# Kernel optimization log

Measured on AMD Instinct MI355X. Metric: run time of the kernel, lower is better.

## Reference

```python
import jax, jax.numpy as jnp
import numpy as np

E = 16      # number of encoders
L = 3       # RNN blocks per encoder
D_IN = 32   # input feature dim
D = 512     # RNN state dim
H_FF = 2048 # encoder FFNN hidden
D_ENC = 512 # encoder output dim
N_DEC = 4   # decoder layers
H_DEC = 2048
D_OUT = 1024
T = 128     # sequence length


def setup_inputs() -> dict:
    key = jax.random.key(0)
    ks = jax.random.split(key, 16)
    def s(k, shape, fan):
        return jax.random.normal(k, shape, jnp.float32) / np.sqrt(fan).astype(np.float32)
    return {
        "x": jax.random.normal(ks[0], (1, T, D_IN), jnp.float32),
        "W_in0": s(ks[1], (E, D_IN, D), D_IN),
        "Wh0": s(ks[2], (E, D, D), D),
        "b0": jnp.zeros((E, D), jnp.float32),
        "W_in_rest": s(ks[3], (E, L - 1, D, D), D),
        "Wh_rest": s(ks[4], (E, L - 1, D, D), D),
        "b_rest": jnp.zeros((E, L - 1, D), jnp.float32),
        "W_ff1": s(ks[5], (E, L * D, H_FF), L * D),
        "b_ff1": jnp.zeros((E, H_FF), jnp.float32),
        "W_ff2": s(ks[6], (E, H_FF, D_ENC), H_FF),
        "b_ff2": jnp.zeros((E, D_ENC), jnp.float32),
        "W_d0": s(ks[7], (E * D_ENC, H_DEC), E * D_ENC),
        "b_d0": jnp.zeros((H_DEC,), jnp.float32),
        "W_dmid": s(ks[8], (N_DEC - 2, H_DEC, H_DEC), H_DEC),
        "b_dmid": jnp.zeros((N_DEC - 2, H_DEC), jnp.float32),
        "W_dout": s(ks[9], (H_DEC, D_OUT), H_DEC),
        "b_dout": jnp.zeros((D_OUT,), jnp.float32),
    }


def reference(x, W_in0, Wh0, b0, W_in_rest, Wh_rest, b_rest,
              W_ff1, b_ff1, W_ff2, b_ff2,
              W_d0, b_d0, W_dmid, b_dmid, W_dout, b_dout):
    def step(h, x_t):
        # h: [E, L, D] stacked-RNN states for all 16 encoders; x_t: [D_IN]
        h0 = jnp.tanh(jnp.einsum('i,eid->ed', x_t, W_in0)
                      + jnp.einsum('ed,edk->ek', h[:, 0], Wh0) + b0)
        hs = [h0]
        for l in range(1, L):  # chain blocks: input = previous block's new state
            hl = jnp.tanh(jnp.einsum('ed,edk->ek', hs[-1], W_in_rest[:, l - 1])
                          + jnp.einsum('ed,edk->ek', h[:, l], Wh_rest[:, l - 1])
                          + b_rest[:, l - 1])
            hs.append(hl)
        h_new = jnp.stack(hs, axis=1)                    # [E, L, D]
        cat = h_new.reshape(E, L * D)                    # cat(states, dim=-1)
        ff = jax.nn.gelu(jnp.einsum('ef,efh->eh', cat, W_ff1) + b_ff1)
        enc_out = jnp.einsum('eh,ehk->ek', ff, W_ff2) + b_ff2  # [E, D_ENC]
        # decoder over concatenated encoder outputs
        z = jnp.tanh(enc_out.reshape(-1) @ W_d0 + b_d0)
        for i in range(N_DEC - 2):
            z = jnp.tanh(z @ W_dmid[i] + b_dmid[i])
        y = z @ W_dout + b_dout                          # [D_OUT]
        return h_new, y

    h_init = jnp.zeros((E, L, D), x.dtype)
    _, ys = jax.lax.scan(step, h_init, x[0])             # [T, D_OUT]
    return ys[None]                                      # [1, T, D_OUT]
```

## Files before the change

kernel.cpp:

```cpp
#include <hip/hip_runtime.h>
#include <hip/hip_bf16.h>
#include <hip/hip_fp16.h>

#define E_ 16
#define T_ 128

typedef _Float16 h2_t __attribute__((ext_vector_type(2)));

__device__ __forceinline__ float fdot2u(uint32_t w, uint32_t h, float acc) {
#if __has_builtin(__builtin_amdgcn_fdot2)
  return __builtin_amdgcn_fdot2(__builtin_bit_cast(h2_t, w),
                                __builtin_bit_cast(h2_t, h), acc, false);
#else
  h2_t wv = __builtin_bit_cast(h2_t, w), hv = __builtin_bit_cast(h2_t, h);
  return acc + (float)wv.x * (float)hv.x + (float)wv.y * (float)hv.y;
#endif
}

__device__ __forceinline__ uint32_t rdlane(uint32_t v, int l) {
  return (uint32_t)__builtin_amdgcn_readlane((int)v, l);
}

__device__ __forceinline__ uint32_t packh2(float a, float b) {
  h2_t p; p.x = (_Float16)a; p.y = (_Float16)b;
  return __builtin_bit_cast(uint32_t, p);
}

__device__ __forceinline__ float apply_act(float v, int act) {
  if (act == 1) return tanhf(v);
  if (act == 2) {
    const float c = 0.7978845608028654f;
    return 0.5f * v * (1.0f + tanhf(c * (v + 0.044715f * v * v * v)));
  }
  return v;
}

__global__ void __launch_bounds__(256) gemm_skinny(
    const float* __restrict__ A, const float* __restrict__ W,
    const float* __restrict__ bias, float* __restrict__ C, float* __restrict__ part,
    int N, int K, int lda, int ldc,
    long sAe, long sWe, long sBe, long sCe,
    int S, int act)
{
  int n0 = blockIdx.x * 64;
  int e  = blockIdx.y;
  int s  = blockIdx.z;
  const float* Ae = A + (long)e * sAe;
  const float* We = W + (long)e * sWe + n0;
  int kper = K / S;
  int kb = s * kper, ke = kb + kper;

  __shared__ float As[32][132];
  __shared__ float Ws[32][68];
  int tid = threadIdx.x;
  int tn = tid & 15, tm = tid >> 4;
  float acc[8][4];
  #pragma unroll
  for (int i = 0; i < 8; ++i)
    #pragma unroll
    for (int j = 0; j < 4; ++j) acc[i][j] = 0.f;

  for (int k0 = kb; k0 < ke; k0 += 32) {
    #pragma unroll
    for (int i = 0; i < 4; ++i) {
      int li = i * 1024 + tid * 4;
      int r = li >> 5, kk = li & 31;
      float4 a4 = *(const float4*)(Ae + (long)r * lda + k0 + kk);
      As[kk+0][r] = a4.x; As[kk+1][r] = a4.y; As[kk+2][r] = a4.z; As[kk+3][r] = a4.w;
    }
    #pragma unroll
    for (int i = 0; i < 2; ++i) {
      int li = i * 1024 + tid * 4;
      int kk = li >> 6, j = li & 63;
      *(float4*)&Ws[kk][j] = *(const float4*)(We + (long)(k0 + kk) * N + j);
    }
    __syncthreads();
    #pragma unroll
    for (int kk = 0; kk < 32; ++kk) {
      float4 a0 = *(const float4*)&As[kk][tm*8];
      float4 a1 = *(const float4*)&As[kk][tm*8+4];
      float4 w4 = *(const float4*)&Ws[kk][tn*4];
      float av[8] = {a0.x,a0.y,a0.z,a0.w,a1.x,a1.y,a1.z,a1.w};
      float wv[4] = {w4.x,w4.y,w4.z,w4.w};
      #pragma unroll
      for (int i2 = 0; i2 < 8; ++i2)
        #pragma unroll
        for (int j2 = 0; j2 < 4; ++j2)
          acc[i2][j2] = fmaf(av[i2], wv[j2], acc[i2][j2]);
    }
    __syncthreads();
  }

  if (S == 1) {
    #pragma unroll
    for (int i2 = 0; i2 < 8; ++i2) {
      int r = tm * 8 + i2;
      float4 o; float* op = (float*)&o;
      #pragma unroll
      for (int j2 = 0; j2 < 4; ++j2)
        op[j2] = apply_act(acc[i2][j2] + bias[(long)e*sBe + n0 + tn*4 + j2], act);
      *(float4*)(C + (long)e*sCe + (long)r*ldc + n0 + tn*4) = o;
    }
  } else {
    float* pp = part + ((long)(s * gridDim.y + e) * 128) * N;
    #pragma unroll
    for (int i2 = 0; i2 < 8; ++i2) {
      int r = tm * 8 + i2;
      float4 o; float* op = (float*)&o;
      #pragma unroll
      for (int j2 = 0; j2 < 4; ++j2) op[j2] = acc[i2][j2];
      *(float4*)(pp + (long)r * N + n0 + tn*4) = o;
    }
  }
}

__global__ void __launch_bounds__(256) reduce_ep(
    const float* __restrict__ part, const float* __restrict__ bias, float* __restrict__ C,
    int S, int N, int ldc, long sBe, long sCe, int act, int total, int Eb)
{
  int idx = blockIdx.x * 256 + threadIdx.x;
  if (idx >= total) return;
  int n = idx % N;
  int r = (idx / N) & 127;
  int e = idx / (N * 128);
  long sstride = (long)Eb * 128 * N;
  float v = 0.f;
  for (int s = 0; s < S; ++s) v += part[s * sstride + ((long)e * 128 + r) * N + n];
  v = apply_act(v + bias[(long)e * sBe + n], act);
  C[(long)e * sCe + (long)r * ldc + n] = v;
}

#define RNN_NV 46
#define RNN_NG 9

__global__ void
__attribute__((amdgpu_flat_work_group_size(1024, 1024)))
__attribute__((amdgpu_waves_per_eu(4, 4)))
__attribute__((amdgpu_num_vgpr(128)))
rnn_seq(
    const float* __restrict__ P,
    const float* __restrict__ Wh,
    float* __restrict__ H,
    long sWe)
{
  __shared__ uint32_t lw[RNN_NG * 4096];
  __shared__ uint32_t hbuf[256];
  __shared__ float    red[3 * 512];

  int tid  = threadIdx.x;
  int lane = tid & 63;
  int wid  = tid >> 6;
  int kq   = wid >> 2;
  int colg = wid & 3;
  int c0   = colg * 128 + lane * 2;
  int e    = blockIdx.x;

  const float* W = Wh + (long)e * sWe;

  uint32_t w0[RNN_NV], w1[RNN_NV];
  #pragma unroll
  for (int q = 0; q < RNN_NV; ++q) {
    int k = kq * 128 + 2 * q;
    float2 ra = *(const float2*)(W + (long)k * 512 + c0);
    float2 rb = *(const float2*)(W + (long)(k + 1) * 512 + c0);
    w0[q] = packh2(ra.x, rb.x);
    w1[q] = packh2(ra.y, rb.y);
  }
  for (int g = 0; g < RNN_NG; ++g) {
    int k = kq * 128 + 2 * (RNN_NV + 2 * g);
    float2 ra = *(const float2*)(W + (long)(k + 0) * 512 + c0);
    float2 rb = *(const float2*)(W + (long)(k + 1) * 512 + c0);
    float2 rc = *(const float2*)(W + (long)(k + 2) * 512 + c0);
    float2 rd = *(const float2*)(W + (long)(k + 3) * 512 + c0);
    uint4 v;
    v.x = packh2(ra.x, rb.x);
    v.y = packh2(ra.y, rb.y);
    v.z = packh2(rc.x, rd.x);
    v.w = packh2(rc.y, rd.y);
    *(uint4*)(lw + ((long)g * 1024 + tid) * 4) = v;
  }
  if (tid < 256) hbuf[tid] = 0;
  __syncthreads();

  for (int t = 0; t < T_; ++t) {
    float2 pv = make_float2(0.f, 0.f);
    if (kq == 0) pv = *(const float2*)(P + ((long)t * E_ + e) * 512 + c0);
    uint32_t hr = hbuf[kq * 64 + lane];
    float a0 = 0.f, a1 = 0.f;
    #pragma unroll
    for (int L = 0; L < RNN_NV; ++L) {
      uint32_t hb = rdlane(hr, L);
      a0 = fdot2u(w0[L], hb, a0);
      a1 = fdot2u(w1[L], hb, a1);
    }
    #pragma unroll
    for (int g = 0; g < RNN_NG; ++g) {
      uint4 v = *(const uint4*)(lw + (g * 1024 + tid) * 4);
      uint32_t hb0 = rdlane(hr, RNN_NV + 2 * g);
      uint32_t hb1 = rdlane(hr, RNN_NV + 2 * g + 1);
      a0 = fdot2u(v.x, hb0, a0);
      a1 = fdot2u(v.y, hb0, a1);
      a0 = fdot2u(v.z, hb1, a0);
      a1 = fdot2u(v.w, hb1, a1);
    }
    if (kq) *(float2*)(red + (kq - 1) * 512 + c0) = make_float2(a0, a1);
    __syncthreads();
    if (kq == 0) {
      float v0 = a0 + red[c0]     + red[512 + c0]     + red[1024 + c0]     + pv.x;
      float v1 = a1 + red[c0 + 1] + red[512 + c0 + 1] + red[1024 + c0 + 1] + pv.y;
      v0 = tanhf(v0); v1 = tanhf(v1);
      *(float2*)(H + ((long)t * E_ + e) * 1536 + c0) = make_float2(v0, v1);
      hbuf[colg * 64 + lane] = packh2(v0, v1);
    }
    __syncthreads();
  }
}

extern "C" void kernel_launch(void* const* d_in, const int* in_sizes, int n_in,
                              void* d_out, int out_size, void* d_ws, size_t ws_size,
                              hipStream_t stream)
{
  const float* x      = (const float*)d_in[0];
  const float* W_in0  = (const float*)d_in[1];
  const float* Wh0    = (const float*)d_in[2];
  const float* b0     = (const float*)d_in[3];
  const float* W_inr  = (const float*)d_in[4];
  const float* Wh_r   = (const float*)d_in[5];
  const float* b_r    = (const float*)d_in[6];
  const float* W_ff1  = (const float*)d_in[7];
  const float* b_ff1  = (const float*)d_in[8];
  const float* W_ff2  = (const float*)d_in[9];
  const float* b_ff2  = (const float*)d_in[10];
  const float* W_d0   = (const float*)d_in[11];
  const float* b_d0   = (const float*)d_in[12];
  const float* W_dmid = (const float*)d_in[13];
  const float* b_dmid = (const float*)d_in[14];
  const float* W_dout = (const float*)d_in[15];
  const float* b_dout = (const float*)d_in[16];
  float* ws = (float*)d_ws;

  float* h    = ws;
  float* P    = ws + 3145728;
  float* FF   = ws + 4194304;
  float* ENC  = ws + 8388608;
  float* Z0   = ws + 9437184;
  float* Z1   = ws + 9699328;
  float* Z2   = ws + 9961472;
  float* PART = ws + 10223616;

  (void)in_sizes; (void)n_in; (void)out_size; (void)ws_size;

  dim3 blk(256);

  gemm_skinny<<<dim3(8,16,1), blk, 0, stream>>>(x, W_in0, b0, P, PART,
      512, 32, 32, 8192, 0L, 16384L, 512L, 512L, 1, 0);
  rnn_seq<<<dim3(16), dim3(1024), 0, stream>>>(P, Wh0, h, 262144L);
  gemm_skinny<<<dim3(8,16,1), blk, 0, stream>>>(h, W_inr, b_r, P, PART,
      512, 512, 24576, 8192, 1536L, 524288L, 1024L, 512L, 1, 0);
  rnn_seq<<<dim3(16), dim3(1024), 0, stream>>>(P, Wh_r, h + 512, 524288L);
  gemm_skinny<<<dim3(8,16,1), blk, 0, stream>>>(h + 512, W_inr + 262144, b_r + 512, P, PART,
      512, 512, 24576, 8192, 1536L, 524288L, 1024L, 512L, 1, 0);
  rnn_seq<<<dim3(16), dim3(1024), 0, stream>>>(P, Wh_r + 262144, h + 1024, 524288L);
  gemm_skinny<<<dim3(32,16,1), blk, 0, stream>>>(h, W_ff1, b_ff1, FF, PART,
      2048, 1536, 24576, 32768, 1536L, 3145728L, 2048L, 2048L, 1, 2);
  gemm_skinny<<<dim3(8,16,2), blk, 0, stream>>>(FF, W_ff2, b_ff2, ENC, PART,
      512, 2048, 32768, 8192, 2048L, 1048576L, 512L, 512L, 2, 0);
  reduce_ep<<<dim3(4096), blk, 0, stream>>>(PART, b_ff2, ENC,
      2, 512, 8192, 512L, 512L, 0, 16*128*512, 16);
  gemm_skinny<<<dim3(32,1,8), blk, 0, stream>>>(ENC, W_d0, b_d0, Z0, PART,
      2048, 8192, 8192, 2048, 0L, 0L, 0L, 0L, 8, 0);
  reduce_ep<<<dim3(1024), blk, 0, stream>>>(PART, b_d0, Z0,
      8, 2048, 2048, 0L, 0L, 1, 128*2048, 1);
  gemm_skinny<<<dim3(32,1,8), blk, 0, stream>>>(Z0, W_dmid, b_dmid, Z1, PART,
      2048, 2048, 2048, 2048, 0L, 0L, 0L, 0L, 8, 0);
  reduce_ep<<<dim3(1024), blk, 0, stream>>>(PART, b_dmid, Z1,
      8, 2048, 2048, 0L, 0L, 1, 128*2048, 1);
  gemm_skinny<<<dim3(32,1,8), blk, 0, stream>>>(Z1, W_dmid + 4194304, b_dmid + 2048, Z2, PART,
      2048, 2048, 2048, 2048, 0L, 0L, 0L, 0L, 8, 0);
  reduce_ep<<<dim3(1024), blk, 0, stream>>>(PART, b_dmid + 2048, Z2,
      8, 2048, 2048, 0L, 0L, 1, 128*2048, 1);
  gemm_skinny<<<dim3(16,1,8), blk, 0, stream>>>(Z2, W_dout, b_dout, (float*)d_out, PART,
      1024, 2048, 2048, 1024, 0L, 0L, 0L, 0L, 8, 0);
  reduce_ep<<<dim3(512), blk, 0, stream>>>(PART, b_dout, (float*)d_out,
      8, 1024, 1024, 0L, 0L, 0, 128*1024, 1);
}
```

Baseline: 1.400 ms.

## Replace FP32 SIMT skinny GEMM with FP16 MFMA 16x16x32 tiles

Rewrites the batched skinny GEMM to use MFMA f32_16x16x32_f16 instructions. Activations are converted to fp16 and staged in shared memory, while weights are loaded straight from global memory, converted per lane, and no longer staged. Each block now covers a 128x128 tile with four waves of 64x64, so the grid's x dimension is halved. This targets the FP32 FMA cost of the encoder/decoder GEMMs. It costs fp16 rounding of the inputs, plus strided uncoalesced weight loads and scalar output stores.

```diff
diff --git a/kernel.cpp b/kernel.cpp
--- a/kernel.cpp
+++ b/kernel.cpp
@@ -6,6 +6,9 @@
 #define T_ 128
 
 typedef _Float16 h2_t __attribute__((ext_vector_type(2)));
+typedef _Float16 half4_t __attribute__((ext_vector_type(4)));
+typedef _Float16 half8_t __attribute__((ext_vector_type(8)));
+typedef float f32x4 __attribute__((ext_vector_type(4)));
 
 __device__ __forceinline__ float fdot2u(uint32_t w, uint32_t h, float acc) {
 #if __has_builtin(__builtin_amdgcn_fdot2)
@@ -35,82 +38,92 @@
   return v;
 }
 
-__global__ void __launch_bounds__(256) gemm_skinny(
+__global__ void __launch_bounds__(256) gemm_mfma(
     const float* __restrict__ A, const float* __restrict__ W,
     const float* __restrict__ bias, float* __restrict__ C, float* __restrict__ part,
     int N, int K, int lda, int ldc,
     long sAe, long sWe, long sBe, long sCe,
     int S, int act)
 {
-  int n0 = blockIdx.x * 64;
+  int n0 = blockIdx.x * 128;
   int e  = blockIdx.y;
   int s  = blockIdx.z;
   const float* Ae = A + (long)e * sAe;
-  const float* We = W + (long)e * sWe + n0;
+  const float* We = W + (long)e * sWe;
   int kper = K / S;
-  int kb = s * kper, ke = kb + kper;
-
-  __shared__ float As[32][132];
-  __shared__ float Ws[32][68];
-  int tid = threadIdx.x;
-  int tn = tid & 15, tm = tid >> 4;
-  float acc[8][4];
+  int kb = s * kper, ke2 = kb + kper;
+
+  __shared__ _Float16 As[128 * 40];
+
+  int tid  = threadIdx.x;
+  int lane = tid & 63;
+  int w    = tid >> 6;
+  int wm   = (w >> 1) * 64;
+  int wn   = (w & 1) * 64;
+  int l16  = lane & 15;
+  int lk   = lane >> 4;
+
+  f32x4 acc[4][4];
   #pragma unroll
-  for (int i = 0; i < 8; ++i)
-    #pragma unroll
-    for (int j = 0; j < 4; ++j) acc[i][j] = 0.f;
-
-  for (int k0 = kb; k0 < ke; k0 += 32) {
+  for (int i = 0; i < 4; ++i)
+    #pragma unroll
+    for (int j = 0; j < 4; ++j)
+      acc[i][j] = (f32x4){0.f, 0.f, 0.f, 0.f};
+
+  for (int k0 = kb; k0 < ke2; k0 += 32) {
+    __syncthreads();
     #pragma unroll
     for (int i = 0; i < 4; ++i) {
-      int li = i * 1024 + tid * 4;
-      int r = li >> 5, kk = li & 31;
-      float4 a4 = *(const float4*)(Ae + (long)r * lda + k0 + kk);
-      As[kk+0][r] = a4.x; As[kk+1][r] = a4.y; As[kk+2][r] = a4.z; As[kk+3][r] = a4.w;
-    }
-    #pragma unroll
-    for (int i = 0; i < 2; ++i) {
-      int li = i * 1024 + tid * 4;
-      int kk = li >> 6, j = li & 63;
-      *(float4*)&Ws[kk][j] = *(const float4*)(We + (long)(k0 + kk) * N + j);
-    }
-    __syncthreads();
-    #pragma unroll
-    for (int kk = 0; kk < 32; ++kk) {
-      float4 a0 = *(const float4*)&As[kk][tm*8];
-      float4 a1 = *(const float4*)&As[kk][tm*8+4];
-      float4 w4 = *(const float4*)&Ws[kk][tn*4];
-      float av[8] = {a0.x,a0.y,a0.z,a0.w,a1.x,a1.y,a1.z,a1.w};
-      float wv[4] = {w4.x,w4.y,w4.z,w4.w};
-      #pragma unroll
-      for (int i2 = 0; i2 < 8; ++i2)
+      int idx = tid + 256 * i;
+      int row = idx >> 3, k4 = idx & 7;
+      float4 a4 = *(const float4*)(Ae + (long)row * lda + k0 + k4 * 4);
+      half4_t hv;
+      hv.x = (_Float16)a4.x; hv.y = (_Float16)a4.y;
+      hv.z = (_Float16)a4.z; hv.w = (_Float16)a4.w;
+      *(half4_t*)(&As[row * 40 + k4 * 4]) = hv;
+    }
+    __syncthreads();
+    #pragma unroll
+    for (int nt = 0; nt < 4; ++nt) {
+      int ncol = n0 + wn + nt * 16 + l16;
+      const float* Wc = We + (long)(k0 + lk * 8) * N + ncol;
+      half8_t b;
+      #pragma unroll
+      for (int j = 0; j < 8; ++j) b[j] = (_Float16)Wc[(long)j * N];
+      #pragma unroll
+      for (int mt = 0; mt < 4; ++mt) {
+        half8_t a = *(const half8_t*)(&As[(wm + mt * 16 + l16) * 40 + lk * 8]);
+        acc[mt][nt] = __builtin_amdgcn_mfma_f32_16x16x32_f16(a, b, acc[mt][nt], 0, 0, 0);
+      }
+    }
+  }
+
+  if (S == 1) {
+    #pragma unroll
+    for (int mt = 0; mt < 4; ++mt)
+      #pragma unroll
+      for (int nt = 0; nt < 4; ++nt) {
+        int col = n0 + wn + nt * 16 + l16;
+        float bv = bias[(long)e * sBe + col];
         #pragma unroll
-        for (int j2 = 0; j2 < 4; ++j2)
-          acc[i2][j2] = fmaf(av[i2], wv[j2], acc[i2][j2]);
-    }
-    __syncthreads();
-  }
-
-  if (S == 1) {
-    #pragma unroll
-    for (int i2 = 0; i2 < 8; ++i2) {
-      int r = tm * 8 + i2;
-      float4 o; float* op = (float*)&o;
-      #pragma unroll
-      for (int j2 = 0; j2 < 4; ++j2)
-        op[j2] = apply_act(acc[i2][j2] + bias[(long)e*sBe + n0 + tn*4 + j2], act);
-      *(float4*)(C + (long)e*sCe + (long)r*ldc + n0 + tn*4) = o;
-    }
+        for (int r = 0; r < 4; ++r) {
+          int row = wm + mt * 16 + lk * 4 + r;
+          C[(long)e * sCe + (long)row * ldc + col] = apply_act(acc[mt][nt][r] + bv, act);
+        }
+      }
   } else {
     float* pp = part + ((long)(s * gridDim.y + e) * 128) * N;
     #pragma unroll
-    for (int i2 = 0; i2 < 8; ++i2) {
-      int r = tm * 8 + i2;
-      float4 o; float* op = (float*)&o;
-      #pragma unroll
-      for (int j2 = 0; j2 < 4; ++j2) op[j2] = acc[i2][j2];
-      *(float4*)(pp + (long)r * N + n0 + tn*4) = o;
-    }
+    for (int mt = 0; mt < 4; ++mt)
+      #pragma unroll
+      for (int nt = 0; nt < 4; ++nt) {
+        int col = n0 + wn + nt * 16 + l16;
+        #pragma unroll
+        for (int r = 0; r < 4; ++r) {
+          int row = wm + mt * 16 + lk * 4 + r;
+          pp[(long)row * N + col] = acc[mt][nt][r];
+        }
+      }
   }
 }
 
@@ -252,34 +265,34 @@
 
   dim3 blk(256);
 
-  gemm_skinny<<<dim3(8,16,1), blk, 0, stream>>>(x, W_in0, b0, P, PART,
+  gemm_mfma<<<dim3(4,16,1), blk, 0, stream>>>(x, W_in0, b0, P, PART,
       512, 32, 32, 8192, 0L, 16384L, 512L, 512L, 1, 0);
   rnn_seq<<<dim3(16), dim3(1024), 0, stream>>>(P, Wh0, h, 262144L);
-  gemm_skinny<<<dim3(8,16,1), blk, 0, stream>>>(h, W_inr, b_r, P, PART,
+  gemm_mfma<<<dim3(4,16,1), blk, 0, stream>>>(h, W_inr, b_r, P, PART,
       512, 512, 24576, 8192, 1536L, 524288L, 1024L, 512L, 1, 0);
   rnn_seq<<<dim3(16), dim3(1024), 0, stream>>>(P, Wh_r, h + 512, 524288L);
-  gemm_skinny<<<dim3(8,16,1), blk, 0, stream>>>(h + 512, W_inr + 262144, b_r + 512, P, PART,
+  gemm_mfma<<<dim3(4,16,1), blk, 0, stream>>>(h + 512, W_inr + 262144, b_r + 512, P, PART,
       512, 512, 24576, 8192, 1536L, 524288L, 1024L, 512L, 1, 0);
   rnn_seq<<<dim3(16), dim3(1024), 0, stream>>>(P, Wh_r + 262144, h + 1024, 524288L);
-  gemm_skinny<<<dim3(32,16,1), blk, 0, stream>>>(h, W_ff1, b_ff1, FF, PART,
+  gemm_mfma<<<dim3(16,16,1), blk, 0, stream>>>(h, W_ff1, b_ff1, FF, PART,
       2048, 1536, 24576, 32768, 1536L, 3145728L, 2048L, 2048L, 1, 2);
-  gemm_skinny<<<dim3(8,16,2), blk, 0, stream>>>(FF, W_ff2, b_ff2, ENC, PART,
+  gemm_mfma<<<dim3(4,16,2), blk, 0, stream>>>(FF, W_ff2, b_ff2, ENC, PART,
       512, 2048, 32768, 8192, 2048L, 1048576L, 512L, 512L, 2, 0);
   reduce_ep<<<dim3(4096), blk, 0, stream>>>(PART, b_ff2, ENC,
       2, 512, 8192, 512L, 512L, 0, 16*128*512, 16);
-  gemm_skinny<<<dim3(32,1,8), blk, 0, stream>>>(ENC, W_d0, b_d0, Z0, PART,
+  gemm_mfma<<<dim3(16,1,8), blk, 0, stream>>>(ENC, W_d0, b_d0, Z0, PART,
       2048, 8192, 8192, 2048, 0L, 0L, 0L, 0L, 8, 0);
   reduce_ep<<<dim3(1024), blk, 0, stream>>>(PART, b_d0, Z0,
       8, 2048, 2048, 0L, 0L, 1, 128*2048, 1);
-  gemm_skinny<<<dim3(32,1,8), blk, 0, stream>>>(Z0, W_dmid, b_dmid, Z1, PART,
+  gemm_mfma<<<dim3(16,1,8), blk, 0, stream>>>(Z0, W_dmid, b_dmid, Z1, PART,
       2048, 2048, 2048, 2048, 0L, 0L, 0L, 0L, 8, 0);
   reduce_ep<<<dim3(1024), blk, 0, stream>>>(PART, b_dmid, Z1,
       8, 2048, 2048, 0L, 0L, 1, 128*2048, 1);
-  gemm_skinny<<<dim3(32,1,8), blk, 0, stream>>>(Z1, W_dmid + 4194304, b_dmid + 2048, Z2, PART,
+  gemm_mfma<<<dim3(16,1,8), blk, 0, stream>>>(Z1, W_dmid + 4194304, b_dmid + 2048, Z2, PART,
       2048, 2048, 2048, 2048, 0L, 0L, 0L, 0L, 8, 0);
   reduce_ep<<<dim3(1024), blk, 0, stream>>>(PART, b_dmid + 2048, Z2,
       8, 2048, 2048, 0L, 0L, 1, 128*2048, 1);
-  gemm_skinny<<<dim3(16,1,8), blk, 0, stream>>>(Z2, W_dout, b_dout, (float*)d_out, PART,
+  gemm_mfma<<<dim3(8,1,8), blk, 0, stream>>>(Z2, W_dout, b_dout, (float*)d_out, PART,
       1024, 2048, 2048, 1024, 0L, 0L, 0L, 0L, 8, 0);
   reduce_ep<<<dim3(512), blk, 0, stream>>>(PART, b_dout, (float*)d_out,
       8, 1024, 1024, 0L, 0L, 0, 128*1024, 1);
```

Result: faster. 1.192 ms (-14.8%).
